# Performance work log

Hardware: AMD Instinct MI355X
Metric: run time of the kernel (lower is better)

Reference implementation:

```python
import jax, jax.numpy as jnp
import numpy as np

SOFTMAX_TEMP = 0.01  # config['networks']['matcher_block']['softmax_temp']
B, WINDOW, C, N, WIDTH = 2, 2, 64, 400, 256


def setup_inputs() -> dict:
    key = jax.random.key(0)
    k1, k2, k3 = jax.random.split(key, 3)
    BW = B * WINDOW
    keypoint_scores = jax.random.uniform(k1, (BW, 1, N), dtype=jnp.float32)
    keypoint_desc = jax.random.normal(k2, (BW, C, N), dtype=jnp.float32)
    desc_dense = jax.random.normal(k3, (BW, C, WIDTH, WIDTH), dtype=jnp.float32)
    # pairing indices exactly as built in SoftmaxRefMatcher.__init__
    tgt_ids, src_ids = [], []
    for b in range(B):
        for w in range(WINDOW - 1):
            for t in range(w + 1, WINDOW):
                src_ids.append(w + b * WINDOW)
                tgt_ids.append(t + b * WINDOW)
    return {
        "keypoint_scores": keypoint_scores,
        "keypoint_desc": keypoint_desc,
        "desc_dense": desc_dense,
        "tgt_ids": jnp.array(tgt_ids, dtype=jnp.int32),
        "src_ids": jnp.array(src_ids, dtype=jnp.int32),
    }


def _l2_normalize(x):
    # F.normalize(x, dim=1), eps=1e-12
    return x / jnp.maximum(jnp.linalg.norm(x, axis=1, keepdims=True), 1e-12)


def reference(keypoint_scores, keypoint_desc, desc_dense, tgt_ids, src_ids):
    BW, Cdim, H, W = desc_dense.shape
    HW = H * W
    # src_coords_dense: meshgrid('ij') -> coords[k] = (u=k%W, v=k//W)
    hw = jnp.arange(HW)
    coords = jnp.stack([(hw % W).astype(jnp.float32),
                        (hw // W).astype(jnp.float32)], axis=1)  # [HW, 2]

    src_desc = _l2_normalize(desc_dense.reshape(BW, Cdim, HW))[src_ids]  # [P, C, HW]
    tgt_desc = _l2_normalize(keypoint_desc)[tgt_ids]                     # [P, C, N]

    match_vals = jnp.einsum('pcn,pcm->pnm', tgt_desc, src_desc)          # [P, N, HW]
    soft_match = jax.nn.softmax(match_vals / SOFTMAX_TEMP, axis=2)
    pseudo_coords = jnp.einsum('pnm,mk->pnk', soft_match, coords)        # [P, N, 2]

    tgt_scores = keypoint_scores[tgt_ids]
    return pseudo_coords, tgt_scores, tgt_ids, src_ids
```

## Files before the change

### kernel.cpp

```cpp
#include <hip/hip_runtime.h>
#include <math.h>

#define NPAIR  2
#define KDIM   64
#define NKP    400
#define NTILE  28
#define HWPIX  65536
#define MREF   70.0f
#define LOG2E  1.44269504f
#define MBLK   256

#define BFRAG_DW (NPAIR*NTILE*2*2*256)

using frag_ab = __attribute__((ext_vector_type(8))) short;
using f32x4   = __attribute__((ext_vector_type(4))) float;

__device__ __forceinline__ unsigned short f2bf(float f){
    unsigned u = __builtin_bit_cast(unsigned, f);
    u += 0x7fffu + ((u >> 16) & 1u);
    return (unsigned short)(u >> 16);
}
__device__ __forceinline__ float bf2f(unsigned short h){
    unsigned u = ((unsigned)h) << 16;
    return __builtin_bit_cast(float, u);
}

__global__ __launch_bounds__(256) void prep_kernel(
    const float* __restrict__ ksc, const float* __restrict__ kd,
    const int* __restrict__ tgt_ids, const int* __restrict__ src_ids,
    unsigned* __restrict__ wsu, float* __restrict__ out)
{
    __shared__ float xs[KDIM][33];
    __shared__ float inv_s[32];
    int d = blockIdx.x, p = blockIdx.y, t = threadIdx.x;
    int tgt = tgt_ids[p];
    int nl = t & 31, c0 = t >> 5;
    #pragma unroll
    for (int cc = 0; cc < 8; ++cc){
        int c = cc*8 + c0;
        int n = d*32 + nl;
        xs[c][nl] = (n < NKP) ? kd[(tgt*KDIM + c)*NKP + n] : 0.f;
    }
    __syncthreads();
    if (t < 32){
        float s = 0.f;
        #pragma unroll
        for (int c = 0; c < KDIM; ++c){ float v = xs[c][t]; s = fmaf(v, v, s); }
        inv_s[t] = 1.f / fmaxf(sqrtf(s), 1e-12f);
    }
    __syncthreads();
    {
        int l = t & 63, rk = t >> 6;
        int rt = rk >> 1, ks = rk & 1;
        int cl = l & 15, g = l >> 4;
        int nloc = rt*16 + cl;
        float inv = inv_s[nloc];
        int k0 = ks*32 + g*8;
        unsigned hu[4], lu[4];
        #pragma unroll
        for (int j2 = 0; j2 < 4; ++j2){
            float xa = xs[k0 + 2*j2    ][nloc] * inv;
            float xb = xs[k0 + 2*j2 + 1][nloc] * inv;
            unsigned short ha = f2bf(xa), hb = f2bf(xb);
            unsigned short la = f2bf(xa - bf2f(ha)), lb = f2bf(xb - bf2f(hb));
            hu[j2] = (unsigned)ha | ((unsigned)hb << 16);
            lu[j2] = (unsigned)la | ((unsigned)lb << 16);
        }
        int nt = d*2 + rt;
        unsigned base = (unsigned)(((p*NTILE + nt)*2 + ks)*2)*256 + l*4;
        *(uint4*)&wsu[base]       = make_uint4(hu[0], hu[1], hu[2], hu[3]);
        *(uint4*)&wsu[base + 256] = make_uint4(lu[0], lu[1], lu[2], lu[3]);
    }
    if (t < 32){
        int n = d*32 + t;
        if (n < NKP) out[NPAIR*NKP*2 + p*NKP + n] = ksc[tgt*NKP + n];
    }
    if (d == 0 && t == 0){
        out[NPAIR*NKP*3 + p]         = (float)tgt;
        out[NPAIR*NKP*3 + NPAIR + p] = (float)src_ids[p];
    }
}

__global__ __launch_bounds__(256, 2) void match_kernel(
    const float* __restrict__ dd, const int* __restrict__ src_ids,
    const unsigned* __restrict__ wsu, float* __restrict__ part)
{
    __shared__ unsigned lds[8192];
    __shared__ float ssp[256];
    __shared__ float invn_s[256];
    int mb = blockIdx.x, p = blockIdx.y, t = threadIdx.x;
    int w = t >> 6, l = t & 63;
    int g = l >> 4;

    const unsigned* wB = wsu + (unsigned)p*28672 + (unsigned)l*4;
    uint4 Bb0[4], Bb1[4];
    #pragma unroll
    for (int k = 0; k < 4; ++k) Bb0[k] = *(const uint4*)(wB + k*256);
    #pragma unroll
    for (int k = 0; k < 4; ++k) Bb1[k] = *(const uint4*)(wB + 1024 + k*256);

    const float* plane = dd + (size_t)src_ids[p]*KDIM*HWPIX + (size_t)mb*256;

    uint4 Ac[4][4];
    int m = t & 127, kh = t >> 7;
    #pragma unroll
    for (int chunk = 0; chunk < 2; ++chunk){
        unsigned sw = (unsigned)(m & 7);
        float ssum = 0.f;
        const float* cp = plane + chunk*128 + m + (size_t)kh*32*HWPIX;
        #pragma unroll
        for (int s2l = 0; s2l < 4; ++s2l){
            float v[8];
            #pragma unroll
            for (int j = 0; j < 8; ++j) v[j] = cp[(size_t)(s2l*8 + j)*HWPIX];
            unsigned hq[4], lq[4];
            #pragma unroll
            for (int q = 0; q < 4; ++q){
                float a = v[2*q], b = v[2*q+1];
                ssum = fmaf(a, a, ssum);
                ssum = fmaf(b, b, ssum);
                unsigned ta = (__builtin_bit_cast(unsigned, a) + 0x8000u) & 0xFFFF0000u;
                unsigned tb = (__builtin_bit_cast(unsigned, b) + 0x8000u) & 0xFFFF0000u;
                float la = a - __builtin_bit_cast(float, ta);
                float lb = b - __builtin_bit_cast(float, tb);
                hq[q] = __builtin_amdgcn_perm(tb, ta, 0x07060302u);
                lq[q] = __builtin_amdgcn_perm(__builtin_bit_cast(unsigned, lb),
                                              __builtin_bit_cast(unsigned, la), 0x07060302u);
            }
            unsigned slot = ((unsigned)(kh*4 + s2l)) ^ sw;
            unsigned dwb = (unsigned)m*32 + slot*4;
            *(uint4*)&lds[dwb]        = make_uint4(hq[0], hq[1], hq[2], hq[3]);
            *(uint4*)&lds[4096 + dwb] = make_uint4(lq[0], lq[1], lq[2], lq[3]);
        }
        ssp[t] = ssum;
        __syncthreads();
        if (t < 128)
            invn_s[chunk*128 + t] =
                (100.f * LOG2E) / fmaxf(sqrtf(ssp[t] + ssp[t + 128]), 1e-12f);
        if ((w >> 1) == chunk){
            int lw = (w & 1)*64;
            #pragma unroll
            for (int mt = 0; mt < 4; ++mt){
                unsigned mm = (unsigned)(lw + mt*16 + (l & 15));
                unsigned sw2 = mm & 7;
                #pragma unroll
                for (int k = 0; k < 4; ++k){
                    unsigned slot = (((unsigned)(k >> 1))*4 + (unsigned)g) ^ sw2;
                    Ac[mt][k] = *(const uint4*)&lds[(unsigned)(k & 1)*4096 + mm*32 + slot*4];
                }
            }
        }
        __syncthreads();
    }

    const float mref2 = MREF * LOG2E;
    float invm8[4][4], ub_[4];
    int mloc0 = w*64;
    #pragma unroll
    for (int mt = 0; mt < 4; ++mt){
        ub_[mt] = (float)(mloc0 + mt*16 + g*4);
        #pragma unroll
        for (int r = 0; r < 4; ++r)
            invm8[mt][r] = invn_s[mloc0 + mt*16 + g*4 + r];
    }

    f32x4 acc0[4], acc1[4];
    float* wp = (float*)lds;

    auto zacc = [&](f32x4* a){
        #pragma unroll
        for (int mt = 0; mt < 4; ++mt) a[mt] = (f32x4){0.f,0.f,0.f,0.f};
    };
    auto unit = [&](const uint4* Bq, f32x4* a4){
        #pragma unroll
        for (int ks = 0; ks < 2; ++ks){
            frag_ab bH = __builtin_bit_cast(frag_ab, Bq[ks*2]);
            frag_ab bL = __builtin_bit_cast(frag_ab, Bq[ks*2 + 1]);
            #pragma unroll
            for (int mt = 0; mt < 4; ++mt){
                frag_ab aH = __builtin_bit_cast(frag_ab, Ac[mt][ks*2]);
                a4[mt] = __builtin_amdgcn_mfma_f32_16x16x32_bf16(aH, bH, a4[mt], 0, 0, 0);
            }
            #pragma unroll
            for (int mt = 0; mt < 4; ++mt){
                frag_ab aH = __builtin_bit_cast(frag_ab, Ac[mt][ks*2]);
                a4[mt] = __builtin_amdgcn_mfma_f32_16x16x32_bf16(aH, bL, a4[mt], 0, 0, 0);
            }
            #pragma unroll
            for (int mt = 0; mt < 4; ++mt){
                frag_ab aL = __builtin_bit_cast(frag_ab, Ac[mt][ks*2 + 1]);
                a4[mt] = __builtin_amdgcn_mfma_f32_16x16x32_bf16(aL, bH, a4[mt], 0, 0, 0);
            }
        }
    };
    auto loadB = [&](int nt, uint4* B){
        const unsigned* q = wB + (unsigned)nt*1024;
        #pragma unroll
        for (int k = 0; k < 4; ++k) B[k] = *(const uint4*)(q + k*256);
    };
    auto epi = [&](const f32x4* a4, int nt){
        float Ssum = 0.f, Usum = 0.f;
        #pragma unroll
        for (int mt = 0; mt < 4; ++mt){
            float e0 = __builtin_amdgcn_exp2f(fmaf(a4[mt][0], invm8[mt][0], -mref2));
            float e1 = __builtin_amdgcn_exp2f(fmaf(a4[mt][1], invm8[mt][1], -mref2));
            float e2 = __builtin_amdgcn_exp2f(fmaf(a4[mt][2], invm8[mt][2], -mref2));
            float e3 = __builtin_amdgcn_exp2f(fmaf(a4[mt][3], invm8[mt][3], -mref2));
            float Sm = (e0 + e1) + (e2 + e3);
            float Um = fmaf(e2, 2.f, e1);
            Um = fmaf(e3, 3.f, Um);
            Um = fmaf(ub_[mt], Sm, Um);
            Ssum += Sm; Usum += Um;
        }
        Ssum += __shfl_xor(Ssum, 16); Usum += __shfl_xor(Usum, 16);
        Ssum += __shfl_xor(Ssum, 32); Usum += __shfl_xor(Usum, 32);
        if (l < 16)
            *(float2*)&wp[((unsigned)(w*NTILE + nt)*16 + (unsigned)l)*2] =
                make_float2(Ssum, Usum);
    };

    zacc(acc0); unit(Bb0, acc0);
    #pragma unroll 1
    for (int jj = 0; jj < 13; ++jj){
        loadB(2*jj + 2, Bb0);
        zacc(acc1); unit(Bb1, acc1);
        epi(acc0, 2*jj);
        loadB(2*jj + 3, Bb1);
        zacc(acc0); unit(Bb0, acc0);
        epi(acc1, 2*jj + 1);
    }
    zacc(acc1); unit(Bb1, acc1);
    epi(acc0, 26);
    epi(acc1, 27);

    __syncthreads();
    for (int idx = t; idx < NTILE*16; idx += 256){
        int nt = idx >> 4, cl = idx & 15;
        float S = 0.f, U = 0.f;
        #pragma unroll
        for (int ww = 0; ww < 4; ++ww){
            float2 q = *(const float2*)&wp[((unsigned)(ww*NTILE + nt)*16 + (unsigned)cl)*2];
            S += q.x; U += q.y;
        }
        *(float2*)&part[(((size_t)p*NTILE + nt)*MBLK + mb)*32 + cl*2] =
            make_float2(S, U);
    }
}

__global__ __launch_bounds__(256) void merge_kernel(
    const float* __restrict__ part, float* __restrict__ out)
{
    __shared__ float red[3][4][16];
    int nt = blockIdx.x, p = blockIdx.y, t = threadIdx.x;
    int j = t & 15, mb0 = t >> 4;
    const float* base = part + (size_t)(p*NTILE + nt)*MBLK*32;
    float S = 0.f, U = 0.f, V = 0.f;
    #pragma unroll 4
    for (int k = 0; k < 16; ++k){
        int mbk = mb0 + k*16;
        float2 q = *(const float2*)&base[(mbk*16 + j)*2];
        S += q.x;
        U += q.y;
        V = fmaf((float)mbk, q.x, V);
    }
    S += __shfl_xor(S, 16); U += __shfl_xor(U, 16); V += __shfl_xor(V, 16);
    S += __shfl_xor(S, 32); U += __shfl_xor(U, 32); V += __shfl_xor(V, 32);
    int w = t >> 6, l = t & 63;
    if (l < 16){ red[0][w][j] = S; red[1][w][j] = U; red[2][w][j] = V; }
    __syncthreads();
    if (t < 16){
        float Sf = red[0][0][t] + red[0][1][t] + red[0][2][t] + red[0][3][t];
        float Uf = red[1][0][t] + red[1][1][t] + red[1][2][t] + red[1][3][t];
        float Vf = red[2][0][t] + red[2][1][t] + red[2][2][t] + red[2][3][t];
        int n = nt*16 + t;
        out[(p*NKP + n)*2 + 0] = Uf / Sf;
        out[(p*NKP + n)*2 + 1] = Vf / Sf;
    }
}

extern "C" void kernel_launch(void* const* d_in, const int* in_sizes, int n_in,
                              void* d_out, int out_size, void* d_ws, size_t ws_size,
                              hipStream_t stream)
{
    const float* ksc     = (const float*)d_in[0];
    const float* kd      = (const float*)d_in[1];
    const float* dd      = (const float*)d_in[2];
    const int*   tgt_ids = (const int*)d_in[3];
    const int*   src_ids = (const int*)d_in[4];
    float* out = (float*)d_out;
    unsigned* wsu = (unsigned*)d_ws;
    float* part = (float*)d_ws + BFRAG_DW;

    prep_kernel <<<dim3(14, NPAIR),   256, 0, stream>>>(ksc, kd, tgt_ids, src_ids, wsu, out);
    match_kernel<<<dim3(MBLK, NPAIR), 256, 0, stream>>>(dd, src_ids, wsu, part);
    merge_kernel<<<dim3(25, NPAIR),   256, 0, stream>>>(part, out);
}
```

Baseline: 126.0 us.

## Load A fragments directly from global into registers, bypassing LDS staging

Each wave now loads its own 64-pixel slice of the dense descriptor straight into MFMA A-fragment layout and converts it in registers. It computes the per-pixel L2 norms with cross-lane shuffles instead of shared-memory partial sums. This drops the LDS staging buffers and both block-wide barriers, and shrinks shared memory use, which may allow more resident blocks. The trade-off is a less coalesced global access pattern: each lane reads 16 contiguous pixels per channel row rather than 128.

Result: no change. 126.0 us (-0.0%).

```diff
diff --git a/kernel.cpp b/kernel.cpp
--- a/kernel.cpp
+++ b/kernel.cpp
@@ -85,12 +85,10 @@
     const float* __restrict__ dd, const int* __restrict__ src_ids,
     const unsigned* __restrict__ wsu, float* __restrict__ part)
 {
-    __shared__ unsigned lds[8192];
-    __shared__ float ssp[256];
-    __shared__ float invn_s[256];
+    __shared__ float wp[4*NTILE*16*2];
     int mb = blockIdx.x, p = blockIdx.y, t = threadIdx.x;
     int w = t >> 6, l = t & 63;
-    int g = l >> 4;
+    int g = l >> 4, c15 = l & 15;
 
     const unsigned* wB = wsu + (unsigned)p*28672 + (unsigned)l*4;
     uint4 Bb0[4], Bb1[4];
@@ -99,24 +97,28 @@
     #pragma unroll
     for (int k = 0; k < 4; ++k) Bb1[k] = *(const uint4*)(wB + 1024 + k*256);
 
-    const float* plane = dd + (size_t)src_ids[p]*KDIM*HWPIX + (size_t)mb*256;
+    const float* plane = dd + (size_t)src_ids[p]*KDIM*HWPIX;
+    int wbase = mb*256 + w*64;
 
     uint4 Ac[4][4];
-    int m = t & 127, kh = t >> 7;
-    #pragma unroll
-    for (int chunk = 0; chunk < 2; ++chunk){
-        unsigned sw = (unsigned)(m & 7);
+    float invv[4];
+    #pragma unroll
+    for (int mt = 0; mt < 4; ++mt){
+        const float* ap = plane + (size_t)(g*8)*HWPIX
+                        + (unsigned)(wbase + mt*16 + c15);
+        float v[2][8];
+        #pragma unroll
+        for (int ks = 0; ks < 2; ++ks)
+            #pragma unroll
+            for (int j = 0; j < 8; ++j)
+                v[ks][j] = ap[(size_t)(ks*32 + j)*HWPIX];
         float ssum = 0.f;
-        const float* cp = plane + chunk*128 + m + (size_t)kh*32*HWPIX;
-        #pragma unroll
-        for (int s2l = 0; s2l < 4; ++s2l){
-            float v[8];
-            #pragma unroll
-            for (int j = 0; j < 8; ++j) v[j] = cp[(size_t)(s2l*8 + j)*HWPIX];
+        #pragma unroll
+        for (int ks = 0; ks < 2; ++ks){
             unsigned hq[4], lq[4];
             #pragma unroll
             for (int q = 0; q < 4; ++q){
-                float a = v[2*q], b = v[2*q+1];
+                float a = v[ks][2*q], b = v[ks][2*q+1];
                 ssum = fmaf(a, a, ssum);
                 ssum = fmaf(b, b, ssum);
                 unsigned ta = (__builtin_bit_cast(unsigned, a) + 0x8000u) & 0xFFFF0000u;
@@ -127,45 +129,24 @@
                 lq[q] = __builtin_amdgcn_perm(__builtin_bit_cast(unsigned, lb),
                                               __builtin_bit_cast(unsigned, la), 0x07060302u);
             }
-            unsigned slot = ((unsigned)(kh*4 + s2l)) ^ sw;
-            unsigned dwb = (unsigned)m*32 + slot*4;
-            *(uint4*)&lds[dwb]        = make_uint4(hq[0], hq[1], hq[2], hq[3]);
-            *(uint4*)&lds[4096 + dwb] = make_uint4(lq[0], lq[1], lq[2], lq[3]);
-        }
-        ssp[t] = ssum;
-        __syncthreads();
-        if (t < 128)
-            invn_s[chunk*128 + t] =
-                (100.f * LOG2E) / fmaxf(sqrtf(ssp[t] + ssp[t + 128]), 1e-12f);
-        if ((w >> 1) == chunk){
-            int lw = (w & 1)*64;
-            #pragma unroll
-            for (int mt = 0; mt < 4; ++mt){
-                unsigned mm = (unsigned)(lw + mt*16 + (l & 15));
-                unsigned sw2 = mm & 7;
-                #pragma unroll
-                for (int k = 0; k < 4; ++k){
-                    unsigned slot = (((unsigned)(k >> 1))*4 + (unsigned)g) ^ sw2;
-                    Ac[mt][k] = *(const uint4*)&lds[(unsigned)(k & 1)*4096 + mm*32 + slot*4];
-                }
-            }
-        }
-        __syncthreads();
-    }
-
+            Ac[mt][ks*2    ] = make_uint4(hq[0], hq[1], hq[2], hq[3]);
+            Ac[mt][ks*2 + 1] = make_uint4(lq[0], lq[1], lq[2], lq[3]);
+        }
+        ssum += __shfl_xor(ssum, 16);
+        ssum += __shfl_xor(ssum, 32);
+        invv[mt] = (100.f * LOG2E) / fmaxf(sqrtf(ssum), 1e-12f);
+    }
     const float mref2 = MREF * LOG2E;
     float invm8[4][4], ub_[4];
-    int mloc0 = w*64;
     #pragma unroll
     for (int mt = 0; mt < 4; ++mt){
-        ub_[mt] = (float)(mloc0 + mt*16 + g*4);
+        ub_[mt] = (float)(w*64 + mt*16 + g*4);
         #pragma unroll
         for (int r = 0; r < 4; ++r)
-            invm8[mt][r] = invn_s[mloc0 + mt*16 + g*4 + r];
+            invm8[mt][r] = __shfl(invv[mt], (l & 48) | (g*4 + r));
     }
 
     f32x4 acc0[4], acc1[4];
-    float* wp = (float*)lds;
 
     auto zacc = [&](f32x4* a){
         #pragma unroll
```
